# Performance work log

Measured on AMD Instinct MI355X. Metric: run time of the kernel, lower is better.

## Reference

```python
import jax, jax.numpy as jnp
import numpy as np

BSZ, MAXQ, DH = 64, 32, 300
N_ENT, N_REL, N_TRI = 100000, 18, 600000
NUM_STEPS = 3
D_CLS = 1024


def setup_inputs() -> dict:
    key = jax.random.key(0)
    ks = jax.random.split(key, 20)
    s = 1.0 / np.sqrt(DH)
    inp = {
        "q_word_h": jax.random.normal(ks[0], (BSZ, MAXQ, DH), jnp.float32),
        "q_embeddings": jax.random.normal(ks[1], (BSZ, DH), jnp.float32),
        "e_s": jax.random.uniform(ks[2], (BSZ, N_ENT), jnp.float32),
        # per-step encoders: Linear(300,300)+Tanh, stacked over steps
        "W_step": jax.random.normal(ks[3], (NUM_STEPS, DH, DH), jnp.float32) * s,
        "b_step": jnp.zeros((NUM_STEPS, DH), jnp.float32),
        "W_cq": jax.random.normal(ks[4], (2 * DH, DH), jnp.float32) * s,
        "b_cq": jnp.zeros((DH,), jnp.float32),
        "W_ca": jax.random.normal(ks[5], (DH,), jnp.float32) * s,
        "b_ca": jnp.zeros((), jnp.float32),
        "W_rel": jax.random.normal(ks[6], (DH, N_REL), jnp.float32) * s,
        "b_rel": jnp.zeros((N_REL,), jnp.float32),
        "ent_emb": jax.random.normal(ks[7], (N_ENT, DH), jnp.float32) * s,
        "W_e1": jax.random.normal(ks[8], (DH, D_CLS), jnp.float32) * s,
        "b_e1": jnp.zeros((D_CLS,), jnp.float32),
        "W_e2": jax.random.normal(ks[9], (D_CLS, N_ENT), jnp.float32) / np.sqrt(D_CLS),
        "b_e2": jnp.zeros((N_ENT,), jnp.float32),
        # sparse KG triple lists (Msubj/Mrel/Mobj one-hot selectors)
        "subj_idx": jax.random.randint(ks[10], (N_TRI,), 0, N_ENT, jnp.int32),
        "rel_idx": jax.random.randint(ks[11], (N_TRI,), 0, N_REL, jnp.int32),
        "obj_idx": jax.random.randint(ks[12], (N_TRI,), 0, N_ENT, jnp.int32),
    }
    return inp


def _follow(e, r, subj_idx, rel_idx, obj_idx):
    # x[t, b] = e[b, subj[t]] * r[b, rel[t]];  out[b, o] = sum_{t: obj[t]=o} x[t, b]
    x = jnp.take(e, subj_idx, axis=1) * jnp.take(r, rel_idx, axis=1)  # [bsz, n_tri]
    return jax.ops.segment_sum(x.T, obj_idx, num_segments=N_ENT).T    # [bsz, n_ent]


def reference(q_word_h, q_embeddings, e_s, W_step, b_step, W_cq, b_cq, W_ca, b_ca,
              W_rel, b_rel, ent_emb, W_e1, b_e1, W_e2, b_e2,
              subj_idx, rel_idx, obj_idx):
    last_e = e_s
    last_c = jnp.zeros((q_word_h.shape[0], DH), q_word_h.dtype)
    for t in range(NUM_STEPS):
        q_t = jnp.tanh(q_embeddings @ W_step[t] + b_step[t])                 # [b, d]
        cq_t = jnp.concatenate([last_c, q_t], axis=1) @ W_cq + b_cq          # [b, d]
        # ca_linear((cq_t[:,None,:] * q_word_h)) -> logits over words
        q_logits = jnp.einsum('bd,bqd,d->bq', cq_t, q_word_h, W_ca) + b_ca   # [b, q]
        q_dist = jax.nn.softmax(q_logits, axis=1)
        last_c = jnp.einsum('bq,bqd->bd', q_dist, q_word_h)                  # attended ctx
        rel_dist = jax.nn.softmax(last_c @ W_rel + b_rel, axis=1)            # [b, n_rel]
        last_e = _follow(last_e, rel_dist, subj_idx, rel_idx, obj_idx)       # [b, n_ent]
    normed = last_e / (jnp.sum(last_e, axis=1, keepdims=True) + 1e-6)
    pred_e = normed @ ent_emb                                                # [b, d]
    pred_e = jnp.maximum(pred_e @ W_e1 + b_e1, 0.0) @ W_e2 + b_e2            # [b, n_ent]
    return pred_e
```

## Files before the change

kernel.cpp:

```cpp
#include <hip/hip_runtime.h>
#include <cstdint>

#define BSZ   64
#define MAXQ  32
#define DH    300
#define N_ENT 100000
#define N_REL 18
#define N_TRI 600000
#define D_CLS 1024

__global__ __launch_bounds__(256) void k_transpose(const float* __restrict__ e_s,
                                                   float* __restrict__ e_t) {
  __shared__ float T[64][65];
  int e0 = blockIdx.x * 64;
  int lane = threadIdx.x & 63;
  int w = threadIdx.x >> 6;
  for (int b = w; b < 64; b += 4) {
    int e = e0 + lane;
    T[b][lane] = (e < N_ENT) ? e_s[b * N_ENT + e] : 0.f;
  }
  __syncthreads();
  for (int i = w; i < 64; i += 4) {
    int e = e0 + i;
    if (e < N_ENT) e_t[e * 64 + lane] = T[lane][i];
  }
}

__global__ __launch_bounds__(320) void k_step(
    const float* __restrict__ qwh, const float* __restrict__ qemb,
    const float* __restrict__ Wstep, const float* __restrict__ bstep,
    const float* __restrict__ Wcq, const float* __restrict__ bcq,
    const float* __restrict__ Wca, const float* __restrict__ bca,
    const float* __restrict__ Wrel, const float* __restrict__ brel,
    float* __restrict__ last_c, float* __restrict__ rel_dist, int t) {
  int b = blockIdx.x;
  int tid = threadIdx.x;
  __shared__ float qe[DH], qtL[DH], lcL[DH], wcq[DH];
  __shared__ float lg[MAXQ], red[MAXQ * 8], dist[MAXQ];
  __shared__ float relL[N_REL];
  __shared__ float mx, sm;

  for (int j = tid; j < DH; j += 320) {
    qe[j] = qemb[b * DH + j];
    lcL[j] = last_c[b * DH + j];
  }
  __syncthreads();

  const float* Wt = Wstep + t * DH * DH;
  for (int j = tid; j < DH; j += 320) {
    float acc = bstep[t * DH + j];
    for (int k = 0; k < DH; k++) acc += qe[k] * Wt[k * DH + j];
    qtL[j] = tanhf(acc);
  }
  __syncthreads();

  for (int j = tid; j < DH; j += 320) {
    float acc = bcq[j];
    for (int k = 0; k < DH; k++) acc += lcL[k] * Wcq[k * DH + j];
    for (int k = 0; k < DH; k++) acc += qtL[k] * Wcq[(DH + k) * DH + j];
    wcq[j] = acc * Wca[j];
  }
  __syncthreads();

  if (tid < MAXQ * 8) {
    int q = tid >> 3, sub = tid & 7;
    const float* row = qwh + (b * MAXQ + q) * DH;
    float acc = 0.f;
    for (int d = sub; d < DH; d += 8) acc += wcq[d] * row[d];
    red[tid] = acc;
  }
  __syncthreads();
  if (tid < MAXQ) {
    float acc = bca[0];
    for (int s = 0; s < 8; s++) acc += red[tid * 8 + s];
    lg[tid] = acc;
  }
  __syncthreads();
  if (tid == 0) {
    float m = lg[0];
    for (int q = 1; q < MAXQ; q++) m = fmaxf(m, lg[q]);
    mx = m;
  }
  __syncthreads();
  if (tid < MAXQ) dist[tid] = expf(lg[tid] - mx);
  __syncthreads();
  if (tid == 0) {
    float s = 0.f;
    for (int q = 0; q < MAXQ; q++) s += dist[q];
    sm = s;
  }
  __syncthreads();

  for (int j = tid; j < DH; j += 320) {
    float acc = 0.f;
    for (int q = 0; q < MAXQ; q++) acc += dist[q] * qwh[(b * MAXQ + q) * DH + j];
    acc /= sm;
    lcL[j] = acc;
    last_c[b * DH + j] = acc;
  }
  __syncthreads();

  if (tid < N_REL) {
    float acc = brel[tid];
    for (int d = 0; d < DH; d++) acc += lcL[d] * Wrel[d * N_REL + tid];
    relL[tid] = acc;
  }
  __syncthreads();
  if (tid == 0) {
    float m = relL[0];
    for (int r = 1; r < N_REL; r++) m = fmaxf(m, relL[r]);
    mx = m;
  }
  __syncthreads();
  if (tid < N_REL) relL[tid] = expf(relL[tid] - mx);
  __syncthreads();
  if (tid == 0) {
    float s = 0.f;
    for (int r = 0; r < N_REL; r++) s += relL[r];
    sm = s;
  }
  __syncthreads();
  if (tid < N_REL) rel_dist[b * N_REL + tid] = relL[tid] / sm;
}

__global__ __launch_bounds__(256) void k_follow(
    const float* __restrict__ e_in, const float* __restrict__ rel_dist,
    const int* __restrict__ subj, const int* __restrict__ rel,
    const int* __restrict__ obj, float* __restrict__ e_out,
    float* __restrict__ sums) {
  __shared__ float relL[BSZ * N_REL];
  for (int i = threadIdx.x; i < BSZ * N_REL; i += 256) relL[i] = rel_dist[i];
  __syncthreads();
  int lane = threadIdx.x & 63;
  int wave = (blockIdx.x << 2) | (threadIdx.x >> 6);
  int nwaves = gridDim.x << 2;
  float sacc = 0.f;
  for (int i = wave; i < N_TRI; i += nwaves) {
    int s = subj[i], r = rel[i], o = obj[i];
    float x = e_in[s * 64 + lane] * relL[lane * N_REL + r];
    sacc += x;
    atomicAdd(&e_out[o * 64 + lane], x);
  }
  if (sums) atomicAdd(&sums[lane], sacc);
}

#define PF_NB 512
#define PF_EPB 196
#define PF_CH 32
#define PF_RS 304
__global__ __launch_bounds__(256) void k_predfeat(
    const float* __restrict__ e, const float* __restrict__ sums,
    const float* __restrict__ ent_emb, float* __restrict__ partials) {
  __shared__ float embL[PF_CH * PF_RS];
  __shared__ float eL[PF_CH * 64];
  int tid = threadIdx.x;
  int b = tid & 63, g = tid >> 6;
  int e0 = blockIdx.x * PF_EPB;
  int e1 = e0 + PF_EPB;
  if (e1 > N_ENT) e1 = N_ENT;

  int sb = (4 * tid) & 63;
  float4 inv4 = make_float4(1.f / (sums[sb + 0] + 1e-6f), 1.f / (sums[sb + 1] + 1e-6f),
                            1.f / (sums[sb + 2] + 1e-6f), 1.f / (sums[sb + 3] + 1e-6f));

  float4 acc[19];
  #pragma unroll
  for (int k = 0; k < 19; k++) acc[k] = make_float4(0.f, 0.f, 0.f, 0.f);

  float4* embL4 = (float4*)embL;
  float4* eL4 = (float4*)eL;

  for (int ecur = e0; ecur < e1; ecur += PF_CH) {
    int n = min(PF_CH, e1 - ecur);
    __syncthreads();
    const float4* src = (const float4*)(ent_emb + (size_t)ecur * DH);
    for (int i = tid; i < n * 75; i += 256) {
      int ee = i / 75, j = i - ee * 75;
      embL4[ee * 76 + j] = src[i];
      if (j == 0) embL4[ee * 76 + 75] = make_float4(0.f, 0.f, 0.f, 0.f);
    }
    const float4* esrc = (const float4*)(e + (size_t)ecur * 64);
    for (int i = tid; i < n * 16; i += 256) {
      float4 v = esrc[i];
      v.x *= inv4.x; v.y *= inv4.y; v.z *= inv4.z; v.w *= inv4.w;
      eL4[i] = v;
    }
    __syncthreads();
    for (int ee = 0; ee < n; ee++) {
      float ev = eL[ee * 64 + b];
      const float4* em = embL4 + ee * 76 + g * 19;
      #pragma unroll
      for (int k = 0; k < 19; k++) {
        float4 m = em[k];
        acc[k].x += ev * m.x;
        acc[k].y += ev * m.y;
        acc[k].z += ev * m.z;
        acc[k].w += ev * m.w;
      }
    }
  }

  float* pout = partials + (size_t)blockIdx.x * (PF_RS * 64);
  #pragma unroll
  for (int k = 0; k < 19; k++) {
    int d = g * 76 + k * 4;
    pout[(d + 0) * 64 + b] = acc[k].x;
    pout[(d + 1) * 64 + b] = acc[k].y;
    pout[(d + 2) * 64 + b] = acc[k].z;
    pout[(d + 3) * 64 + b] = acc[k].w;
  }
}

__global__ __launch_bounds__(256) void k_reduce_pf(const float* __restrict__ partials,
                                                   float* __restrict__ pf) {
  int j = blockIdx.x * 256 + threadIdx.x;
  if (j >= DH * 64) return;
  int d = j >> 6, b = j & 63;
  float acc = 0.f;
  for (int c = 0; c < PF_NB; c++) acc += partials[(size_t)c * (PF_RS * 64) + j];
  pf[b * DH + d] = acc;
}

__global__ __launch_bounds__(256) void k_hidden(const float* __restrict__ pf,
                                                const float* __restrict__ We1,
                                                const float* __restrict__ be1,
                                                float* __restrict__ hiddenT) {
  int idx = blockIdx.x * 256 + threadIdx.x;
  int j = idx & (D_CLS - 1);
  int b = idx >> 10;
  float acc = be1[j];
  const float* p = pf + b * DH;
  for (int k = 0; k < DH; k++) acc += p[k] * We1[k * D_CLS + j];
  hiddenT[j * 64 + b] = fmaxf(acc, 0.f);
}

#define FO_TILE 512
__global__ __launch_bounds__(256) void k_final(const float* __restrict__ hT,
                                               const float* __restrict__ We2,
                                               const float* __restrict__ be2,
                                               float* __restrict__ out) {
  int tid = threadIdx.x;
  int o0 = blockIdx.x * FO_TILE + tid * 2;
  int bg = blockIdx.y * 16;
  bool valid = (o0 < N_ENT);
  int oc = valid ? o0 : 0;

  float2 acc[16];
  #pragma unroll
  for (int i = 0; i < 16; i++) acc[i] = make_float2(0.f, 0.f);

  const float* h = hT + bg;
  const float* w = We2 + oc;
  #pragma unroll 4
  for (int k = 0; k < D_CLS; k++) {
    float2 wv = *(const float2*)(w + (size_t)k * N_ENT);
    const float* hk = h + k * 64;
    #pragma unroll
    for (int i = 0; i < 16; i++) {
      acc[i].x += hk[i] * wv.x;
      acc[i].y += hk[i] * wv.y;
    }
  }

  if (valid) {
    float2 bv = *(const float2*)(be2 + oc);
    #pragma unroll
    for (int i = 0; i < 16; i++) {
      float2 v = make_float2(acc[i].x + bv.x, acc[i].y + bv.y);
      *(float2*)(out + (size_t)(bg + i) * N_ENT + o0) = v;
    }
  }
}

extern "C" void kernel_launch(void* const* d_in, const int* in_sizes, int n_in,
                              void* d_out, int out_size, void* d_ws, size_t ws_size,
                              hipStream_t stream) {
  const float* qwh   = (const float*)d_in[0];
  const float* qemb  = (const float*)d_in[1];
  const float* e_s   = (const float*)d_in[2];
  const float* Wstep = (const float*)d_in[3];
  const float* bstep = (const float*)d_in[4];
  const float* Wcq   = (const float*)d_in[5];
  const float* bcq   = (const float*)d_in[6];
  const float* Wca   = (const float*)d_in[7];
  const float* bca   = (const float*)d_in[8];
  const float* Wrel  = (const float*)d_in[9];
  const float* brel  = (const float*)d_in[10];
  const float* eemb  = (const float*)d_in[11];
  const float* We1   = (const float*)d_in[12];
  const float* be1   = (const float*)d_in[13];
  const float* We2   = (const float*)d_in[14];
  const float* be2   = (const float*)d_in[15];
  const int* subj    = (const int*)d_in[16];
  const int* rel     = (const int*)d_in[17];
  const int* obj     = (const int*)d_in[18];
  float* out = (float*)d_out;

  float* ws = (float*)d_ws;
  const size_t EB = (size_t)N_ENT * 64;
  float* eb0     = ws;
  float* eb1     = ws + EB;
  float* eb2     = ws + 2 * EB;
  float* eb3     = ws + 3 * EB;
  float* last_c  = ws + 4 * EB;
  float* sums    = last_c + BSZ * DH;
  float* rel_d   = sums + 64;
  float* pf      = rel_d + BSZ * N_REL;
  float* hiddenT = pf + BSZ * DH;
  float* partials = eb1;

  hipMemsetAsync(last_c, 0, (size_t)(BSZ * DH + 64) * sizeof(float), stream);
  hipMemsetAsync(eb1, 0, 3 * EB * sizeof(float), stream);

  k_transpose<<<(N_ENT + 63) / 64, 256, 0, stream>>>(e_s, eb0);

  float* chain[4] = {eb0, eb1, eb2, eb3};
  for (int t = 0; t < 3; t++) {
    k_step<<<BSZ, 320, 0, stream>>>(qwh, qemb, Wstep, bstep, Wcq, bcq, Wca, bca,
                                    Wrel, brel, last_c, rel_d, t);
    k_follow<<<2048, 256, 0, stream>>>(chain[t], rel_d, subj, rel, obj, chain[t + 1],
                                       (t == 2) ? sums : nullptr);
  }

  k_predfeat<<<PF_NB, 256, 0, stream>>>(eb3, sums, eemb, partials);
  k_reduce_pf<<<(DH * 64 + 255) / 256, 256, 0, stream>>>(partials, pf);
  k_hidden<<<(BSZ * D_CLS) / 256, 256, 0, stream>>>(pf, We1, be1, hiddenT);
  dim3 fgrid((N_ENT + FO_TILE - 1) / FO_TILE, 4);
  k_final<<<fgrid, 256, 0, stream>>>(hiddenT, We2, be2, out);
}
```

Before: 1.730 ms.

## Build CSR by object per call and replace atomic scatter with gather in follow

Each call now builds a CSR grouping of triples by object (histogram, two-pass scan, atomic scatter of subject and relation packed into one word). The follow kernel then gathers per destination entity and writes each output row once, so it no longer issues an atomicAdd per triple per lane and no longer needs the zeroed output buffers. The CSR build adds several small kernels and 600k atomics on every call. Per-wave work also becomes uneven because entities have different in-degrees.

```diff
diff --git a/kernel.cpp b/kernel.cpp
--- a/kernel.cpp
+++ b/kernel.cpp
@@ -23,6 +23,64 @@
   for (int i = w; i < 64; i += 4) {
     int e = e0 + i;
     if (e < N_ENT) e_t[e * 64 + lane] = T[lane][i];
+  }
+}
+
+__global__ __launch_bounds__(256) void k_hist(const int* __restrict__ obj,
+                                              int* __restrict__ cnt) {
+  int stride = gridDim.x * 256;
+  for (int i = blockIdx.x * 256 + threadIdx.x; i < N_TRI; i += stride)
+    atomicAdd(&cnt[obj[i]], 1);
+}
+
+__global__ __launch_bounds__(256) void k_scan1(const int* __restrict__ cnt,
+                                               int* __restrict__ cursor,
+                                               int* __restrict__ blockSums) {
+  __shared__ int sdata[256];
+  int i = blockIdx.x * 256 + threadIdx.x;
+  int v = (i < N_ENT) ? cnt[i] : 0;
+  sdata[threadIdx.x] = v;
+  __syncthreads();
+  for (int off = 1; off < 256; off <<= 1) {
+    int t = (threadIdx.x >= off) ? sdata[threadIdx.x - off] : 0;
+    __syncthreads();
+    sdata[threadIdx.x] += t;
+    __syncthreads();
+  }
+  if (i < N_ENT) cursor[i] = sdata[threadIdx.x] - v;
+  if (threadIdx.x == 255) blockSums[blockIdx.x] = sdata[255];
+}
+
+__global__ __launch_bounds__(256) void k_scan2(const int* __restrict__ blockSums,
+                                               int* __restrict__ rowStart,
+                                               int* __restrict__ cursor) {
+  __shared__ int offs;
+  int b = blockIdx.x;
+  if (threadIdx.x == 0) {
+    int o = 0;
+    for (int j = 0; j < b; j++) o += blockSums[j];
+    offs = o;
+  }
+  __syncthreads();
+  int i = b * 256 + threadIdx.x;
+  if (i < N_ENT) {
+    int v = cursor[i] + offs;
+    rowStart[i] = v;
+    cursor[i] = v;
+  }
+  if (i == 0) rowStart[N_ENT] = N_TRI;
+}
+
+__global__ __launch_bounds__(256) void k_scatter(const int* __restrict__ subj,
+                                                 const int* __restrict__ rel,
+                                                 const int* __restrict__ obj,
+                                                 int* __restrict__ cursor,
+                                                 uint32_t* __restrict__ packed) {
+  int stride = gridDim.x * 256;
+  for (int i = blockIdx.x * 256 + threadIdx.x; i < N_TRI; i += stride) {
+    int o = obj[i];
+    int pos = atomicAdd(&cursor[o], 1);
+    packed[pos] = (uint32_t)subj[i] | ((uint32_t)rel[i] << 17);
   }
 }
 
@@ -125,21 +183,30 @@
 
 __global__ __launch_bounds__(256) void k_follow(
     const float* __restrict__ e_in, const float* __restrict__ rel_dist,
-    const int* __restrict__ subj, const int* __restrict__ rel,
-    const int* __restrict__ obj, float* __restrict__ e_out,
-    float* __restrict__ sums) {
-  __shared__ float relL[BSZ * N_REL];
-  for (int i = threadIdx.x; i < BSZ * N_REL; i += 256) relL[i] = rel_dist[i];
+    const int* __restrict__ rowStart, const uint32_t* __restrict__ packed,
+    float* __restrict__ e_out, float* __restrict__ sums) {
+  __shared__ float relL[BSZ * 19];
+  for (int i = threadIdx.x; i < BSZ * N_REL; i += 256) {
+    int l = i / N_REL, r = i - l * N_REL;
+    relL[l * 19 + r] = rel_dist[i];
+  }
   __syncthreads();
   int lane = threadIdx.x & 63;
   int wave = (blockIdx.x << 2) | (threadIdx.x >> 6);
   int nwaves = gridDim.x << 2;
+  const float* myrel = relL + lane * 19;
   float sacc = 0.f;
-  for (int i = wave; i < N_TRI; i += nwaves) {
-    int s = subj[i], r = rel[i], o = obj[i];
-    float x = e_in[s * 64 + lane] * relL[lane * N_REL + r];
-    sacc += x;
-    atomicAdd(&e_out[o * 64 + lane], x);
+  for (int o = wave; o < N_ENT; o += nwaves) {
+    int beg = rowStart[o], end = rowStart[o + 1];
+    float acc = 0.f;
+    for (int t = beg; t < end; ++t) {
+      uint32_t p = packed[t];
+      int s = p & 0x1FFFF;
+      int r = p >> 17;
+      acc += e_in[s * 64 + lane] * myrel[r];
+    }
+    e_out[(size_t)o * 64 + lane] = acc;
+    sacc += acc;
   }
   if (sums) atomicAdd(&sums[lane], sacc);
 }
@@ -298,31 +365,42 @@
 
   float* ws = (float*)d_ws;
   const size_t EB = (size_t)N_ENT * 64;
-  float* eb0     = ws;
-  float* eb1     = ws + EB;
-  float* eb2     = ws + 2 * EB;
-  float* eb3     = ws + 3 * EB;
-  float* last_c  = ws + 4 * EB;
-  float* sums    = last_c + BSZ * DH;
-  float* rel_d   = sums + 64;
-  float* pf      = rel_d + BSZ * N_REL;
-  float* hiddenT = pf + BSZ * DH;
-  float* partials = eb1;
+  float* e_a      = ws;
+  float* e_b      = e_a + EB;
+  float* partials = e_b + EB;
+  float* last_c   = partials + (size_t)PF_NB * PF_RS * 64;
+  float* sums     = last_c + BSZ * DH;
+  float* rel_d    = sums + 64;
+  float* pf       = rel_d + BSZ * N_REL;
+  float* hiddenT  = pf + BSZ * DH;
+  int* cnt        = (int*)(hiddenT + BSZ * D_CLS);
+  int* rowStart   = cnt + N_ENT;
+  int* cursor     = rowStart + N_ENT + 1;
+  int* blockSums  = cursor + N_ENT;
+  uint32_t* packed = (uint32_t*)(blockSums + 400);
 
   hipMemsetAsync(last_c, 0, (size_t)(BSZ * DH + 64) * sizeof(float), stream);
-  hipMemsetAsync(eb1, 0, 3 * EB * sizeof(float), stream);
-
-  k_transpose<<<(N_ENT + 63) / 64, 256, 0, stream>>>(e_s, eb0);
-
-  float* chain[4] = {eb0, eb1, eb2, eb3};
+  hipMemsetAsync(cnt, 0, (size_t)N_ENT * sizeof(int), stream);
+
+  k_transpose<<<(N_ENT + 63) / 64, 256, 0, stream>>>(e_s, e_a);
+
+  k_hist<<<1024, 256, 0, stream>>>(obj, cnt);
+  int nsb = (N_ENT + 255) / 256;
+  k_scan1<<<nsb, 256, 0, stream>>>(cnt, cursor, blockSums);
+  k_scan2<<<nsb, 256, 0, stream>>>(blockSums, rowStart, cursor);
+  k_scatter<<<1024, 256, 0, stream>>>(subj, rel, obj, cursor, packed);
+
+  float* cur = e_a;
+  float* nxt = e_b;
   for (int t = 0; t < 3; t++) {
     k_step<<<BSZ, 320, 0, stream>>>(qwh, qemb, Wstep, bstep, Wcq, bcq, Wca, bca,
                                     Wrel, brel, last_c, rel_d, t);
-    k_follow<<<2048, 256, 0, stream>>>(chain[t], rel_d, subj, rel, obj, chain[t + 1],
+    k_follow<<<2048, 256, 0, stream>>>(cur, rel_d, rowStart, packed, nxt,
                                        (t == 2) ? sums : nullptr);
-  }
-
-  k_predfeat<<<PF_NB, 256, 0, stream>>>(eb3, sums, eemb, partials);
+    float* tmp = cur; cur = nxt; nxt = tmp;
+  }
+
+  k_predfeat<<<PF_NB, 256, 0, stream>>>(cur, sums, eemb, partials);
   k_reduce_pf<<<(DH * 64 + 255) / 256, 256, 0, stream>>>(partials, pf);
   k_hidden<<<(BSZ * D_CLS) / 256, 256, 0, stream>>>(pf, We1, be1, hiddenT);
   dim3 fgrid((N_ENT + FO_TILE - 1) / FO_TILE, 4);
```

Measured after the change: 1.572 ms. 9.1% less time.
